# Kernel optimization log

Measured on AMD Instinct MI355X. Metric: run time of the kernel, lower is better.

The kernel has to match this reference:

```python
import jax, jax.numpy as jnp
import numpy as np

N_NODES = 100000
N_EDGES = 1600000


def setup_inputs() -> dict:
    key = jax.random.key(0)
    ks = jax.random.split(key, 6)
    x = jax.random.normal(ks[0], (N_NODES, 166), dtype=jnp.float32)
    edge_index = jax.random.randint(ks[1], (2, N_EDGES), 0, N_NODES, dtype=jnp.int64)
    s = 0.05
    return {
        "x": x,
        "edge_index": edge_index,
        "W1l": jax.random.normal(ks[2], (166, 128), dtype=jnp.float32) * s,
        "b1": jnp.zeros((128,), dtype=jnp.float32),
        "W1r": jax.random.normal(ks[3], (166, 128), dtype=jnp.float32) * s,
        "W2l": jax.random.normal(ks[4], (128, 2), dtype=jnp.float32) * s,
        "b2": jnp.zeros((2,), dtype=jnp.float32),
        "W2r": jax.random.normal(ks[5], (128, 2), dtype=jnp.float32) * s,
    }


def _sage_mean_agg(h, src, dst, n_nodes):
    # mean over incoming edges (PyG SAGEConv default aggr='mean');
    # nodes with no in-edges get zeros.
    summed = jax.ops.segment_sum(h[src], dst, num_segments=n_nodes)
    deg = jax.ops.segment_sum(jnp.ones_like(dst, dtype=h.dtype), dst,
                              num_segments=n_nodes)
    return summed / jnp.maximum(deg, 1.0)[:, None]


def reference(x, edge_index, W1l, b1, W1r, W2l, b2, W2r):
    src, dst = edge_index[0], edge_index[1]
    n = x.shape[0]
    # layer 1: out = lin_l(mean_agg(x)) + lin_r(x)
    agg1 = _sage_mean_agg(x, src, dst, n)
    h = agg1 @ W1l + b1 + x @ W1r
    h = jax.nn.relu(h)
    # dropout p=0.5 is identity in eval mode
    # layer 2
    agg2 = _sage_mean_agg(h, src, dst, n)
    out = agg2 @ W2l + b2 + h @ W2r
    return jax.nn.log_softmax(out, axis=1)
```

## Files before the change

kernel.cpp:

```cpp
#include <hip/hip_runtime.h>
#include <hip/hip_bf16.h>
#include <math.h>

#define N_NODES 100000
#define N_EDGES 1600000
#define FDIM 166
#define HDIM 128
#define KP 192
#define CAP 48
#define MBLK 64
#define NXCD 8
#define NODES_PER (N_NODES / NXCD)

typedef __attribute__((ext_vector_type(8))) short bf16x8;
typedef __attribute__((ext_vector_type(4))) float f32x4;

__device__ inline float bf2f(unsigned short s) {
    unsigned int u = ((unsigned int)s) << 16;
    float f; __builtin_memcpy(&f, &u, 4); return f;
}
__device__ inline float bflo(unsigned int u) {
    unsigned int v = u << 16;
    float f; __builtin_memcpy(&f, &v, 4); return f;
}
__device__ inline float bfhi(unsigned int u) {
    unsigned int v = u & 0xffff0000u;
    float f; __builtin_memcpy(&f, &v, 4); return f;
}
__device__ inline unsigned short f2bf(float f) {
    unsigned int u; __builtin_memcpy(&u, &f, 4);
    unsigned int r = u + 0x7fffu + ((u >> 16) & 1u);
    return (unsigned short)(r >> 16);
}
__device__ inline bf16x8 pack8(float4 a, float4 b) {
    union { bf16x8 v; __hip_bfloat162 h[4]; } u;
    u.h[0] = __float22bfloat162_rn(make_float2(a.x, a.y));
    u.h[1] = __float22bfloat162_rn(make_float2(a.z, a.w));
    u.h[2] = __float22bfloat162_rn(make_float2(b.x, b.y));
    u.h[3] = __float22bfloat162_rn(make_float2(b.z, b.w));
    return u.v;
}

__global__ void k_pre(const float* __restrict__ W1l, const float* __restrict__ W1r,
                      unsigned short* __restrict__ wt2, int* __restrict__ cnt) {
    int idx = blockIdx.x * 256 + threadIdx.x;
    if (blockIdx.x < 192) {
        int fb = idx >> 9, r = idx & 511;
        int lane = r >> 3, j = r & 7;
        int g = lane >> 4, l15 = lane & 15;
        int kk = fb / 16, cb = fb & 15;
        int c = cb * 16 + l15;
        int k = kk * 32 + 8 * g + j;
        float v = 0.f;
        if (k < FDIM)
            v = (c < HDIM) ? W1l[k * HDIM + c] : W1r[k * HDIM + (c - HDIM)];
        wt2[idx] = f2bf(v);
    } else {
        int i = idx - 192 * 256;
        if (i < N_NODES) cnt[i] = 0;
    }
}

__global__ __launch_bounds__(256) void k_fill(const int* __restrict__ ei,
                                              int* __restrict__ cnt,
                                              int* __restrict__ adj) {
    int xcd = blockIdx.x & (NXCD - 1);
    int grp = blockIdx.x >> 3;
    int lo = xcd * NODES_PER, hi = lo + NODES_PER;
    int stride = (gridDim.x >> 3) * 256;
    for (int e = grp * 256 + threadIdx.x; e < N_EDGES; e += stride) {
        int d = ei[N_EDGES + e];
        int s = ei[e];
        if (d >= lo && d < hi) {
            int slot = atomicAdd(&cnt[d], 1);
            if (slot < CAP) adj[d * CAP + slot] = s;
        }
    }
}

__global__ __launch_bounds__(256, 3) void k_gemm(
        const float* __restrict__ x, const unsigned short* __restrict__ wt2,
        unsigned short* __restrict__ yl, unsigned short* __restrict__ yr) {
    int tid = threadIdx.x;
    int r0 = blockIdx.x * MBLK;
    int w = tid >> 6, lane = tid & 63;

    int rbase = (w >> 1) * 32;
    int half = w & 1;
    int l15 = lane & 15, g = lane >> 4;

    int gr0 = r0 + rbase + l15;       if (gr0 > N_NODES - 1) gr0 = N_NODES - 1;
    int gr1 = gr0 + 16;               if (gr1 > N_NODES - 1) gr1 = N_NODES - 1;
    const char* xr0 = (const char*)x + (size_t)gr0 * (FDIM * 4) + 32 * g;
    const char* xr1 = (const char*)x + (size_t)gr1 * (FDIM * 4) + 32 * g;

    f32x4 acc[2][8];
    #pragma unroll
    for (int a = 0; a < 2; a++)
        #pragma unroll
        for (int b = 0; b < 8; b++) acc[a][b] = (f32x4){0.f, 0.f, 0.f, 0.f};

    const char* wb = (const char*)wt2 + (size_t)lane * 16;

    for (int kk = 0; kk < 6; ++kk) {
        bf16x8 ww[8];
        #pragma unroll
        for (int cf = 0; cf < 8; cf++)
            ww[cf] = *(const bf16x8*)(wb + (size_t)(kk * 16 + half * 8 + cf) * 1024);
        float4 p0, q0, p1, q1;
        if (kk < 5) {
            p0 = *(const float4*)(xr0 + kk * 128);
            q0 = *(const float4*)(xr0 + kk * 128 + 16);
            p1 = *(const float4*)(xr1 + kk * 128);
            q1 = *(const float4*)(xr1 + kk * 128 + 16);
        } else {
            if (g == 0) {
                p0 = *(const float4*)(xr0 + 640);
                p1 = *(const float4*)(xr1 + 640);
                float2 t0 = *(const float2*)(xr0 + 656);
                float2 t1 = *(const float2*)(xr1 + 656);
                q0 = make_float4(t0.x, t0.y, 0.f, 0.f);
                q1 = make_float4(t1.x, t1.y, 0.f, 0.f);
            } else {
                p0 = make_float4(0.f, 0.f, 0.f, 0.f);
                q0 = p0; p1 = p0; q1 = p0;
            }
        }
        bf16x8 xb0 = pack8(p0, q0);
        bf16x8 xb1 = pack8(p1, q1);
        #pragma unroll
        for (int cf = 0; cf < 8; cf++) {
            acc[0][cf] = __builtin_amdgcn_mfma_f32_16x16x32_bf16(ww[cf], xb0, acc[0][cf], 0, 0, 0);
            acc[1][cf] = __builtin_amdgcn_mfma_f32_16x16x32_bf16(ww[cf], xb1, acc[1][cf], 0, 0, 0);
        }
    }

    unsigned short* dst = half ? yr : yl;
    #pragma unroll
    for (int rf = 0; rf < 2; rf++) {
        int gr = r0 + rbase + 16 * rf + l15;
        if (gr < N_NODES) {
            #pragma unroll
            for (int cf = 0; cf < 8; cf++) {
                ushort4 o;
                o.x = f2bf(acc[rf][cf][0]); o.y = f2bf(acc[rf][cf][1]);
                o.z = f2bf(acc[rf][cf][2]); o.w = f2bf(acc[rf][cf][3]);
                *(ushort4*)&dst[(size_t)gr * HDIM + 16 * cf + 4 * g] = o;
            }
        }
    }
}

__global__ __launch_bounds__(256) void k_agg1(
        const unsigned short* __restrict__ yl, const unsigned short* __restrict__ yr,
        const int* __restrict__ cnt, const int* __restrict__ adj,
        const float* __restrict__ b1,
        const float* __restrict__ W2l, const float* __restrict__ W2r,
        float* __restrict__ zw) {
    int w = threadIdx.x >> 6, lane = threadIdx.x & 63;
    int i = blockIdx.x * 4 + w;
    if (i >= N_NODES) return;
    int deg = cnt[i];
    int n = min(deg, CAP);
    int aidx = adj[i * CAP + lane];
    float a0 = 0.f, a1 = 0.f, p0 = 0.f, p1 = 0.f, q0 = 0.f, q1 = 0.f, r0 = 0.f, r1 = 0.f;
    int j = 0;
    for (; j + 4 <= n; j += 4) {
        int s0 = __shfl(aidx, j, 64);
        int s1 = __shfl(aidx, j + 1, 64);
        int s2 = __shfl(aidx, j + 2, 64);
        int s3 = __shfl(aidx, j + 3, 64);
        unsigned int u0 = *(const unsigned int*)&yl[(size_t)s0 * HDIM + lane * 2];
        unsigned int u1 = *(const unsigned int*)&yl[(size_t)s1 * HDIM + lane * 2];
        unsigned int u2 = *(const unsigned int*)&yl[(size_t)s2 * HDIM + lane * 2];
        unsigned int u3 = *(const unsigned int*)&yl[(size_t)s3 * HDIM + lane * 2];
        a0 += bflo(u0); a1 += bfhi(u0);
        p0 += bflo(u1); p1 += bfhi(u1);
        q0 += bflo(u2); q1 += bfhi(u2);
        r0 += bflo(u3); r1 += bfhi(u3);
    }
    for (; j < n; ++j) {
        int s = __shfl(aidx, j, 64);
        unsigned int u = *(const unsigned int*)&yl[(size_t)s * HDIM + lane * 2];
        a0 += bflo(u); a1 += bfhi(u);
    }
    a0 += p0 + q0 + r0;
    a1 += p1 + q1 + r1;
    float inv = 1.f / (float)max(deg, 1);
    unsigned int ur = *(const unsigned int*)&yr[(size_t)i * HDIM + lane * 2];
    float2 bb = *(const float2*)&b1[lane * 2];
    float h0 = fmaxf(a0 * inv + bflo(ur) + bb.x, 0.f);
    float h1 = fmaxf(a1 * inv + bfhi(ur) + bb.y, 0.f);
    float4 wl2 = *(const float4*)&W2l[lane * 4];
    float4 wr2 = *(const float4*)&W2r[lane * 4];
    float z0 = h0 * wl2.x + h1 * wl2.z;
    float z1 = h0 * wl2.y + h1 * wl2.w;
    float w0 = h0 * wr2.x + h1 * wr2.z;
    float w1 = h0 * wr2.y + h1 * wr2.w;
    #pragma unroll
    for (int m = 32; m; m >>= 1) {
        z0 += __shfl_xor(z0, m, 64); z1 += __shfl_xor(z1, m, 64);
        w0 += __shfl_xor(w0, m, 64); w1 += __shfl_xor(w1, m, 64);
    }
    if (lane == 0) {
        float4 o = {z0, z1, w0, w1};
        *(float4*)&zw[i * 4] = o;
    }
}

__global__ void k_out(const float* __restrict__ zw, const int* __restrict__ cnt,
                      const int* __restrict__ adj, const float* __restrict__ b2,
                      float* __restrict__ out) {
    int i = blockIdx.x * 256 + threadIdx.x;
    if (i >= N_NODES) return;
    int deg = cnt[i];
    int n = min(deg, CAP);
    float s0 = 0.f, s1 = 0.f;
    const int* arow = adj + i * CAP;
    for (int j = 0; j < n; j++) {
        int s = arow[j];
        float2 zz = *(const float2*)&zw[s * 4];
        s0 += zz.x; s1 += zz.y;
    }
    float inv = 1.f / (float)max(deg, 1);
    float p0 = s0 * inv + b2[0] + zw[i * 4 + 2];
    float p1 = s1 * inv + b2[1] + zw[i * 4 + 3];
    float mx = fmaxf(p0, p1);
    float lse = mx + logf(expf(p0 - mx) + expf(p1 - mx));
    out[i * 2 + 0] = p0 - lse;
    out[i * 2 + 1] = p1 - lse;
}

extern "C" void kernel_launch(void* const* d_in, const int* in_sizes, int n_in,
                              void* d_out, int out_size, void* d_ws, size_t ws_size,
                              hipStream_t stream) {
    const float* x   = (const float*)d_in[0];
    const int*   ei  = (const int*)d_in[1];
    const float* W1l = (const float*)d_in[2];
    const float* b1  = (const float*)d_in[3];
    const float* W1r = (const float*)d_in[4];
    const float* W2l = (const float*)d_in[5];
    const float* b2  = (const float*)d_in[6];
    const float* W2r = (const float*)d_in[7];
    float* out = (float*)d_out;

    char* ws = (char*)d_ws;
    size_t off = 0;
    auto alloc = [&](size_t bytes) {
        off = (off + 255) & ~(size_t)255;
        void* p = ws + off;
        off += bytes;
        return p;
    };
    int* cnt            = (int*)alloc((size_t)N_NODES * 4);
    int* adj            = (int*)alloc((size_t)N_NODES * CAP * 4);
    unsigned short* wt2 = (unsigned short*)alloc((size_t)256 * KP * 2);
    unsigned short* yl  = (unsigned short*)alloc((size_t)N_NODES * HDIM * 2);
    unsigned short* yr  = (unsigned short*)alloc((size_t)N_NODES * HDIM * 2);
    float* zw           = (float*)alloc((size_t)N_NODES * 4 * 4);
    (void)ws_size; (void)in_sizes; (void)n_in; (void)out_size;

    k_pre<<<192 + (N_NODES + 255) / 256, 256, 0, stream>>>(W1l, W1r, wt2, cnt);
    k_fill<<<2048, 256, 0, stream>>>(ei, cnt, adj);
    k_gemm<<<(N_NODES + MBLK - 1) / MBLK, 256, 0, stream>>>(x, wt2, yl, yr);
    k_agg1<<<(N_NODES + 3) / 4, 256, 0, stream>>>(yl, yr, cnt, adj, b1, W2l, W2r, zw);
    k_out<<<(N_NODES + 255) / 256, 256, 0, stream>>>(zw, cnt, adj, b2, out);
}
```

Before: 202.0 us.

## Fuse adjacency fill and GEMM into one kernel with interleaved block roles

The edge-bucketing fill and the dense bf16 GEMM are merged into one launch. Their blocks are interleaved in groups of eight, so that the atomic-heavy fill runs at the same time as the MFMA GEMM and one launch gap is removed. The fill grid is halved to 1024 blocks, and they now run under the GEMM's launch bounds and register budget. The zw buffer is split into separate z and w arrays, which makes the k_out gather of neighbour z values denser. The GEMM's k-loop is also fully unrolled.

```diff
diff --git a/kernel.cpp b/kernel.cpp
--- a/kernel.cpp
+++ b/kernel.cpp
@@ -11,6 +11,9 @@
 #define MBLK 64
 #define NXCD 8
 #define NODES_PER (N_NODES / NXCD)
+#define FILLB 1024
+#define GEMMB ((N_NODES + MBLK - 1) / MBLK)
+#define TOTB (GEMMB + FILLB)
 
 typedef __attribute__((ext_vector_type(8))) short bf16x8;
 typedef __attribute__((ext_vector_type(4))) float f32x4;
@@ -61,28 +64,34 @@
     }
 }
 
-__global__ __launch_bounds__(256) void k_fill(const int* __restrict__ ei,
-                                              int* __restrict__ cnt,
-                                              int* __restrict__ adj) {
-    int xcd = blockIdx.x & (NXCD - 1);
-    int grp = blockIdx.x >> 3;
-    int lo = xcd * NODES_PER, hi = lo + NODES_PER;
-    int stride = (gridDim.x >> 3) * 256;
-    for (int e = grp * 256 + threadIdx.x; e < N_EDGES; e += stride) {
-        int d = ei[N_EDGES + e];
-        int s = ei[e];
-        if (d >= lo && d < hi) {
-            int slot = atomicAdd(&cnt[d], 1);
-            if (slot < CAP) adj[d * CAP + slot] = s;
-        }
-    }
-}
-
-__global__ __launch_bounds__(256, 3) void k_gemm(
+__global__ __launch_bounds__(256, 3) void k_fused(
         const float* __restrict__ x, const unsigned short* __restrict__ wt2,
-        unsigned short* __restrict__ yl, unsigned short* __restrict__ yr) {
+        unsigned short* __restrict__ yl, unsigned short* __restrict__ yr,
+        const int* __restrict__ ei, int* __restrict__ cnt, int* __restrict__ adj) {
+    int bid = blockIdx.x;
+    int id; bool isfill;
+    if (bid < 2 * FILLB) {
+        isfill = (bid >> 3) & 1;
+        id = ((bid >> 4) << 3) | (bid & 7);
+    } else { isfill = false; id = bid - FILLB; }
+
+    if (isfill) {
+        int xcd = bid & (NXCD - 1);
+        int lo = xcd * NODES_PER, hi = lo + NODES_PER;
+        int stride = (FILLB >> 3) * 256;
+        for (int e = (id >> 3) * 256 + threadIdx.x; e < N_EDGES; e += stride) {
+            int d = ei[N_EDGES + e];
+            int s = ei[e];
+            if (d >= lo && d < hi) {
+                int slot = atomicAdd(&cnt[d], 1);
+                if (slot < CAP) adj[d * CAP + slot] = s;
+            }
+        }
+        return;
+    }
+
     int tid = threadIdx.x;
-    int r0 = blockIdx.x * MBLK;
+    int r0 = id * MBLK;
     int w = tid >> 6, lane = tid & 63;
 
     int rbase = (w >> 1) * 32;
@@ -102,6 +111,7 @@
 
     const char* wb = (const char*)wt2 + (size_t)lane * 16;
 
+    #pragma unroll
     for (int kk = 0; kk < 6; ++kk) {
         bf16x8 ww[8];
         #pragma unroll
@@ -156,7 +166,7 @@
         const int* __restrict__ cnt, const int* __restrict__ adj,
         const float* __restrict__ b1,
         const float* __restrict__ W2l, const float* __restrict__ W2r,
-        float* __restrict__ zw) {
+        float* __restrict__ zarr, float* __restrict__ warr) {
     int w = threadIdx.x >> 6, lane = threadIdx.x & 63;
     int i = blockIdx.x * 4 + w;
     if (i >= N_NODES) return;
@@ -203,14 +213,14 @@
         w0 += __shfl_xor(w0, m, 64); w1 += __shfl_xor(w1, m, 64);
     }
     if (lane == 0) {
-        float4 o = {z0, z1, w0, w1};
-        *(float4*)&zw[i * 4] = o;
-    }
-}
-
-__global__ void k_out(const float* __restrict__ zw, const int* __restrict__ cnt,
-                      const int* __restrict__ adj, const float* __restrict__ b2,
-                      float* __restrict__ out) {
+        *(float2*)&zarr[i * 2] = make_float2(z0, z1);
+        *(float2*)&warr[i * 2] = make_float2(w0, w1);
+    }
+}
+
+__global__ void k_out(const float* __restrict__ zarr, const float* __restrict__ warr,
+                      const int* __restrict__ cnt, const int* __restrict__ adj,
+                      const float* __restrict__ b2, float* __restrict__ out) {
     int i = blockIdx.x * 256 + threadIdx.x;
     if (i >= N_NODES) return;
     int deg = cnt[i];
@@ -219,12 +229,12 @@
     const int* arow = adj + i * CAP;
     for (int j = 0; j < n; j++) {
         int s = arow[j];
-        float2 zz = *(const float2*)&zw[s * 4];
+        float2 zz = *(const float2*)&zarr[s * 2];
         s0 += zz.x; s1 += zz.y;
     }
     float inv = 1.f / (float)max(deg, 1);
-    float p0 = s0 * inv + b2[0] + zw[i * 4 + 2];
-    float p1 = s1 * inv + b2[1] + zw[i * 4 + 3];
+    float p0 = s0 * inv + b2[0] + warr[i * 2 + 0];
+    float p1 = s1 * inv + b2[1] + warr[i * 2 + 1];
     float mx = fmaxf(p0, p1);
     float lse = mx + logf(expf(p0 - mx) + expf(p1 - mx));
     out[i * 2 + 0] = p0 - lse;
@@ -257,12 +267,12 @@
     unsigned short* wt2 = (unsigned short*)alloc((size_t)256 * KP * 2);
     unsigned short* yl  = (unsigned short*)alloc((size_t)N_NODES * HDIM * 2);
     unsigned short* yr  = (unsigned short*)alloc((size_t)N_NODES * HDIM * 2);
-    float* zw           = (float*)alloc((size_t)N_NODES * 4 * 4);
+    float* zarr         = (float*)alloc((size_t)N_NODES * 2 * 4);
+    float* warr         = (float*)alloc((size_t)N_NODES * 2 * 4);
     (void)ws_size; (void)in_sizes; (void)n_in; (void)out_size;
 
     k_pre<<<192 + (N_NODES + 255) / 256, 256, 0, stream>>>(W1l, W1r, wt2, cnt);
-    k_fill<<<2048, 256, 0, stream>>>(ei, cnt, adj);
-    k_gemm<<<(N_NODES + MBLK - 1) / MBLK, 256, 0, stream>>>(x, wt2, yl, yr);
-    k_agg1<<<(N_NODES + 3) / 4, 256, 0, stream>>>(yl, yr, cnt, adj, b1, W2l, W2r, zw);
-    k_out<<<(N_NODES + 255) / 256, 256, 0, stream>>>(zw, cnt, adj, b2, out);
-}
+    k_fused<<<TOTB, 256, 0, stream>>>(x, wt2, yl, yr, ei, cnt, adj);
+    k_agg1<<<(N_NODES + 3) / 4, 256, 0, stream>>>(yl, yr, cnt, adj, b1, W2l, W2r, zarr, warr);
+    k_out<<<(N_NODES + 255) / 256, 256, 0, stream>>>(zarr, warr, cnt, adj, b2, out);
+}
```

Measured after the change: 242.6 us. +20.1%, slower.
